# Optimization experiments

Hardware: AMD Instinct MI355X
Metric: run time of the kernel (lower is better)

The kernel has to match this reference:

```python
import jax, jax.numpy as jnp
import numpy as np

N = 100000
NUM_CLASSES = 10
EPS = 1e-16
NEG_SLOPE = 0.2


def gat_conv(x, src, dst, W, a_src, a_dst, bias, heads, out_ch, concat):
    # x: [N, F_in]; src/dst: [E] (message flows src -> dst, PyG convention)
    n = x.shape[0]
    h = (x @ W).reshape(n, heads, out_ch)              # [N, H, C]
    al = jnp.sum(h * a_src, axis=-1)                   # [N, H] source attention term
    ar = jnp.sum(h * a_dst, axis=-1)                   # [N, H] target attention term
    e = jax.nn.leaky_relu(al[src] + ar[dst], NEG_SLOPE)  # [E, H]
    # segment softmax over incoming edges of each dst node
    m = jax.ops.segment_max(e, dst, num_segments=n)    # [N, H]
    ex = jnp.exp(e - m[dst])                           # [E, H]
    denom = jax.ops.segment_sum(ex, dst, num_segments=n)  # [N, H]
    alpha = ex / (denom[dst] + EPS)                    # [E, H]
    msg = h[src] * alpha[..., None]                    # [E, H, C]
    out = jax.ops.segment_sum(msg, dst, num_segments=n)   # [N, H, C]
    out = out.reshape(n, heads * out_ch) if concat else out.mean(axis=1)
    return out + bias


def setup_inputs() -> dict:
    key = jax.random.key(0)
    ks = jax.random.split(key, 10)
    F_in, H1, C1 = 512, 8, 8
    x = jax.random.normal(ks[0], (N, F_in), dtype=jnp.float32)
    edge_index = jax.random.randint(ks[1], (2, 1600000), 0, N, dtype=jnp.int64)
    s = 0.05
    return {
        "x": x,
        "edge_index": edge_index,
        "W1": jax.random.normal(ks[2], (F_in, H1 * C1), dtype=jnp.float32) * s,
        "a_src1": jax.random.normal(ks[3], (H1, C1), dtype=jnp.float32) * s,
        "a_dst1": jax.random.normal(ks[4], (H1, C1), dtype=jnp.float32) * s,
        "b1": jnp.zeros((H1 * C1,), dtype=jnp.float32),
        "W2": jax.random.normal(ks[5], (H1 * C1, NUM_CLASSES), dtype=jnp.float32) * s,
        "a_src2": jax.random.normal(ks[6], (1, NUM_CLASSES), dtype=jnp.float32) * s,
        "a_dst2": jax.random.normal(ks[7], (1, NUM_CLASSES), dtype=jnp.float32) * s,
        "b2": jnp.zeros((NUM_CLASSES,), dtype=jnp.float32),
    }


def reference(x, edge_index, W1, a_src1, a_dst1, b1, W2, a_src2, a_dst2, b2):
    # add self-loops (GATConv default add_self_loops=True)
    loops = jnp.arange(N, dtype=edge_index.dtype)
    src = jnp.concatenate([edge_index[0], loops])
    dst = jnp.concatenate([edge_index[1], loops])
    # eval mode: dropout(p=0.6) is identity
    h = gat_conv(x, src, dst, W1, a_src1, a_dst1, b1, heads=8, out_ch=8, concat=True)
    h = jax.nn.elu(h)
    out = gat_conv(h, src, dst, W2, a_src2, a_dst2, b2, heads=1, out_ch=NUM_CLASSES, concat=True)
    return jax.nn.log_softmax(out, axis=1)
```

## Files before the change

kernel.cpp:

```cpp
#include <hip/hip_runtime.h>
#include <math.h>

#define NN 100000
#define NEDGE 1600000
#define NTOT 1700000
#define FIN 512
#define NH1 8
#define NC1 8
#define F1 64
#define NC2 10
#define SLOPE 0.2f
#define EPSF 1e-16f
#define SCAN_BLK 1024
#define NB ((NN + SCAN_BLK - 1) / SCAN_BLK)

typedef short short8 __attribute__((ext_vector_type(8)));
typedef float f32x4 __attribute__((ext_vector_type(4)));

__device__ __forceinline__ float lrelu(float x) { return x > 0.f ? x : SLOPE * x; }
__device__ __forceinline__ float eluf(float x) { return x > 0.f ? x : __expf(x) - 1.f; }

__device__ __forceinline__ unsigned short f2bf_rne(float f) {
    unsigned int u = __float_as_uint(f);
    unsigned int r = (u + 0x7FFFu + ((u >> 16) & 1u)) >> 16;
    return (unsigned short)r;
}
__device__ __forceinline__ float bf2f(unsigned short b) {
    return __uint_as_float(((unsigned int)b) << 16);
}

__global__ void k_init(const float* __restrict__ W, unsigned short* __restrict__ wT,
                       int* __restrict__ cnt)
{
    int i = blockIdx.x * 256 + threadIdx.x;
    if (i < NN) cnt[i] = 1;
    if (i < F1 * FIN) {
        int n = i & 63, k = i >> 6;
        wT[n * FIN + k] = f2bf_rne(W[k * F1 + n]);
    }
}

#define LDA 40

__global__ __launch_bounds__(256) void k_gemm1(const float* __restrict__ x,
                                               const unsigned short* __restrict__ wT,
                                               const float* __restrict__ asrc,
                                               const float* __restrict__ adst,
                                               unsigned short* __restrict__ h1b,
                                               float* __restrict__ al,
                                               float* __restrict__ ar)
{
    __shared__ unsigned short Al[64][LDA];
    __shared__ unsigned short Bl[64][LDA];
    __shared__ float sas[F1], sad[F1];
    const int tid = threadIdx.x;
    const int row0 = blockIdx.x * 64;
    const int w  = tid >> 6;
    const int l  = tid & 63;
    const int lr = l & 15;
    const int lg = l >> 4;
    if (tid < F1) { sas[tid] = asrc[tid]; sad[tid] = adst[tid]; }
    f32x4 acc[4] = {};

    for (int k0 = 0; k0 < FIN; k0 += 32) {
        #pragma unroll
        for (int t2 = 0; t2 < 2; ++t2) {
            int idx = tid + t2 * 256;
            int r = idx >> 3, q = idx & 7;
            int gr = row0 + r;
            float4 v = (gr < NN) ? *(const float4*)(x + (size_t)gr * FIN + k0 + 4 * q)
                                 : make_float4(0.f, 0.f, 0.f, 0.f);
            ushort4 u;
            u.x = f2bf_rne(v.x); u.y = f2bf_rne(v.y);
            u.z = f2bf_rne(v.z); u.w = f2bf_rne(v.w);
            *(ushort4*)&Al[r][4 * q] = u;
        }
        {
            int n = tid >> 2, q = tid & 3;
            *(uint4*)&Bl[n][8 * q] = *(const uint4*)(wT + (size_t)n * FIN + k0 + 8 * q);
        }
        __syncthreads();
        short8 a = *(const short8*)&Al[16 * w + lr][8 * lg];
        #pragma unroll
        for (int nt = 0; nt < 4; ++nt) {
            short8 b = *(const short8*)&Bl[16 * nt + lr][8 * lg];
            acc[nt] = __builtin_amdgcn_mfma_f32_16x16x32_bf16(a, b, acc[nt], 0, 0, 0);
        }
        __syncthreads();
    }
    #pragma unroll
    for (int r = 0; r < 4; ++r) {
        int gr = row0 + 16 * w + 4 * lg + r;
        if (gr < NN) {
            #pragma unroll
            for (int nt = 0; nt < 4; ++nt)
                h1b[(size_t)gr * F1 + 16 * nt + lr] = f2bf_rne(acc[nt][r]);
        }
    }
    float pa[4][4], pd[4][4];
    #pragma unroll
    for (int nt = 0; nt < 4; ++nt) {
        float wa = sas[16 * nt + lr], wd = sad[16 * nt + lr];
        #pragma unroll
        for (int r = 0; r < 4; ++r) {
            float c = acc[nt][r];
            pa[nt][r] = c * wa;
            pd[nt][r] = c * wd;
        }
    }
    #pragma unroll
    for (int d = 1; d <= 4; d <<= 1) {
        #pragma unroll
        for (int nt = 0; nt < 4; ++nt)
            #pragma unroll
            for (int r = 0; r < 4; ++r) {
                pa[nt][r] += __shfl_xor(pa[nt][r], d);
                pd[nt][r] += __shfl_xor(pd[nt][r], d);
            }
    }
    int low3 = lr & 7, hi = lr >> 3;
    if (low3 < 4) {
        int head = 2 * low3 + hi;
        #pragma unroll
        for (int nt = 0; nt < 4; ++nt) {
            if (low3 == nt) {
                #pragma unroll
                for (int r = 0; r < 4; ++r) {
                    int gr = row0 + 16 * w + 4 * lg + r;
                    if (gr < NN) {
                        al[gr * NH1 + head] = pa[nt][r];
                        ar[gr * NH1 + head] = pd[nt][r];
                    }
                }
            }
        }
    }
}

__global__ void k_hist(const int* __restrict__ ei, int* __restrict__ cnt,
                       int* __restrict__ pos)
{
    int e = blockIdx.x * blockDim.x + threadIdx.x;
    if (e >= NEDGE) return;
    pos[e] = atomicAdd(&cnt[ei[NEDGE + e]], 1);
}

__global__ __launch_bounds__(256) void k_scan1(const int* __restrict__ cnt,
                                               int* __restrict__ off,
                                               int* __restrict__ bsum)
{
    __shared__ int s[256];
    int t = threadIdx.x;
    int base = blockIdx.x * SCAN_BLK + t * 4;
    int c0 = (base + 0 < NN) ? cnt[base + 0] : 0;
    int c1 = (base + 1 < NN) ? cnt[base + 1] : 0;
    int c2 = (base + 2 < NN) ? cnt[base + 2] : 0;
    int c3 = (base + 3 < NN) ? cnt[base + 3] : 0;
    int ts = c0 + c1 + c2 + c3;
    s[t] = ts;
    __syncthreads();
    #pragma unroll
    for (int d = 1; d < 256; d <<= 1) {
        int v = (t >= d) ? s[t - d] : 0;
        __syncthreads();
        s[t] += v;
        __syncthreads();
    }
    int run = s[t] - ts;
    if (t == 255) bsum[blockIdx.x] = s[255];
    if (base + 0 < NN) off[base + 0] = run; run += c0;
    if (base + 1 < NN) off[base + 1] = run; run += c1;
    if (base + 2 < NN) off[base + 2] = run; run += c2;
    if (base + 3 < NN) off[base + 3] = run;
}

__global__ void k_scan2(int* __restrict__ bsum, int* __restrict__ off)
{
    __shared__ int s[128];
    int t = threadIdx.x;
    int v = (t < NB) ? bsum[t] : 0;
    s[t] = v;
    __syncthreads();
    #pragma unroll
    for (int d = 1; d < 128; d <<= 1) {
        int w = (t >= d) ? s[t - d] : 0;
        __syncthreads();
        s[t] += w;
        __syncthreads();
    }
    if (t < NB) bsum[t] = s[t] - v;
    if (t == 0) off[NN] = NTOT;
}

__global__ void k_scan3(int* __restrict__ off, const int* __restrict__ bsum,
                        int* __restrict__ esrc)
{
    int i = blockIdx.x * blockDim.x + threadIdx.x;
    if (i >= NN) return;
    int o = off[i] + bsum[i >> 10];
    off[i] = o;
    esrc[o] = i;
}

__global__ void k_scatter(const int* __restrict__ ei, const int* __restrict__ off,
                          const int* __restrict__ pos, int* __restrict__ esrc)
{
    int e = blockIdx.x * blockDim.x + threadIdx.x;
    if (e >= NEDGE) return;
    esrc[off[ei[NEDGE + e]] + pos[e]] = ei[e];
}

__global__ __launch_bounds__(256) void k_agg1(const int* __restrict__ off,
                                              const int* __restrict__ esrc,
                                              const float* __restrict__ al,
                                              const float* __restrict__ ar,
                                              const unsigned short* __restrict__ h1b,
                                              const float* __restrict__ b1,
                                              const float* __restrict__ W2,
                                              const float* __restrict__ as2,
                                              const float* __restrict__ ad2,
                                              float* __restrict__ packed)
{
    __shared__ float s2a[NC2], s2d[NC2];
    int tid = threadIdx.x;
    if (tid < NC2) { s2a[tid] = as2[tid]; s2d[tid] = ad2[tid]; }
    __syncthreads();
    int node = blockIdx.x * 4 + (tid >> 6);
    int lane = tid & 63;
    int h = lane >> 3;
    float b1l = b1[lane];
    float w2r[NC2];
    #pragma unroll
    for (int o = 0; o < NC2; ++o) w2r[o] = W2[lane * NC2 + o];

    int beg = off[node], end = off[node + 1];
    float arn = ar[node * NH1 + h];
    float a0 = 0.f, a1 = 0.f, a2 = 0.f, a3 = 0.f;
    float d0 = 0.f, d1 = 0.f, d2 = 0.f, d3 = 0.f;
    int i = beg;
    for (; i + 3 < end; i += 4) {
        int s0 = esrc[i], s1 = esrc[i + 1], s2 = esrc[i + 2], s3 = esrc[i + 3];
        float e0 = __expf(lrelu(al[s0 * NH1 + h] + arn));
        float e1 = __expf(lrelu(al[s1 * NH1 + h] + arn));
        float e2 = __expf(lrelu(al[s2 * NH1 + h] + arn));
        float e3 = __expf(lrelu(al[s3 * NH1 + h] + arn));
        a0 += bf2f(h1b[(size_t)s0 * F1 + lane]) * e0; d0 += e0;
        a1 += bf2f(h1b[(size_t)s1 * F1 + lane]) * e1; d1 += e1;
        a2 += bf2f(h1b[(size_t)s2 * F1 + lane]) * e2; d2 += e2;
        a3 += bf2f(h1b[(size_t)s3 * F1 + lane]) * e3; d3 += e3;
    }
    for (; i < end; ++i) {
        int s0 = esrc[i];
        float e0 = __expf(lrelu(al[s0 * NH1 + h] + arn));
        a0 += bf2f(h1b[(size_t)s0 * F1 + lane]) * e0; d0 += e0;
    }
    float v = ((a0 + a1) + (a2 + a3)) / (((d0 + d1) + (d2 + d3)) + EPSF);
    float gl = eluf(v + b1l);

    float p[NC2];
    #pragma unroll
    for (int o = 0; o < NC2; ++o) p[o] = gl * w2r[o];
    #pragma unroll
    for (int d = 1; d <= 32; d <<= 1)
        #pragma unroll
        for (int o = 0; o < NC2; ++o) p[o] += __shfl_xor(p[o], d);
    float sa = 0.f, sd = 0.f;
    #pragma unroll
    for (int o = 0; o < NC2; ++o) { sa += p[o] * s2a[o]; sd += p[o] * s2d[o]; }

    float* rec = packed + (size_t)node * 16;
    if (lane < NC2) rec[lane] = p[lane];
    if (lane == 10) rec[10] = sa;
    if (lane == 11) rec[11] = sd;
}

__global__ __launch_bounds__(256) void k_agg2(const int* __restrict__ off,
                                              const int* __restrict__ esrc,
                                              const float* __restrict__ packed,
                                              const float* __restrict__ b2,
                                              float* __restrict__ out)
{
    int node = blockIdx.x * 16 + (threadIdx.x >> 4);
    int li = threadIdx.x & 15;
    int beg = off[node], end = off[node + 1];
    float arn = packed[(size_t)node * 16 + 11];
    float acc = 0.f, acc1 = 0.f, dsum = 0.f, dsum1 = 0.f;
    int i = beg;
    for (; i + 1 < end; i += 2) {
        int s0 = esrc[i], s1 = esrc[i + 1];
        float v0 = (li < 12) ? packed[(size_t)s0 * 16 + li] : 0.f;
        float v1 = (li < 12) ? packed[(size_t)s1 * 16 + li] : 0.f;
        float al0 = __shfl(v0, 10, 16);
        float al1 = __shfl(v1, 10, 16);
        float e0 = __expf(lrelu(al0 + arn));
        float e1 = __expf(lrelu(al1 + arn));
        if (li < NC2) { acc += v0 * e0; acc1 += v1 * e1; }
        dsum += e0; dsum1 += e1;
    }
    if (i < end) {
        int s0 = esrc[i];
        float v0 = (li < 12) ? packed[(size_t)s0 * 16 + li] : 0.f;
        float al0 = __shfl(v0, 10, 16);
        float e0 = __expf(lrelu(al0 + arn));
        if (li < NC2) acc += v0 * e0;
        dsum += e0;
    }
    float z = (li < NC2) ? (acc + acc1) / (dsum + dsum1 + EPSF) + b2[li] : -1e30f;
    float m = z;
    #pragma unroll
    for (int d = 8; d >= 1; d >>= 1) m = fmaxf(m, __shfl_xor(m, d, 16));
    float ex = (li < NC2) ? __expf(z - m) : 0.f;
    float ss = ex;
    #pragma unroll
    for (int d = 8; d >= 1; d >>= 1) ss += __shfl_xor(ss, d, 16);
    float ls = __logf(ss) + m;
    if (li < NC2) out[(size_t)node * NC2 + li] = z - ls;
}

extern "C" void kernel_launch(void* const* d_in, const int* in_sizes, int n_in,
                              void* d_out, int out_size, void* d_ws, size_t ws_size,
                              hipStream_t stream)
{
    const float* x    = (const float*)d_in[0];
    const int*   ei   = (const int*)d_in[1];
    const float* W1   = (const float*)d_in[2];
    const float* as1  = (const float*)d_in[3];
    const float* ad1  = (const float*)d_in[4];
    const float* b1   = (const float*)d_in[5];
    const float* W2   = (const float*)d_in[6];
    const float* as2  = (const float*)d_in[7];
    const float* ad2  = (const float*)d_in[8];
    const float* b2   = (const float*)d_in[9];
    float* out = (float*)d_out;

    char* ws = (char*)d_ws;
    unsigned short* h1b = (unsigned short*)ws;
    unsigned short* wT  = h1b + (size_t)NN * F1;
    float* al1 = (float*)(wT + (size_t)F1 * FIN);
    float* ar1 = al1 + (size_t)NN * NH1;
    float* packed = ar1 + (size_t)NN * NH1;
    int* cnt   = (int*)(packed + (size_t)NN * 16);
    int* off   = cnt + NN;
    int* bsum  = off + NN + 1;
    int* esrc  = bsum + 128;
    int* pos   = esrc + NTOT;

    k_init<<<(NN + 255) / 256, 256, 0, stream>>>(W1, wT, cnt);
    k_gemm1<<<(NN + 63) / 64, 256, 0, stream>>>(x, wT, as1, ad1, h1b, al1, ar1);
    k_hist<<<(NEDGE + 255) / 256, 256, 0, stream>>>(ei, cnt, pos);
    k_scan1<<<NB, 256, 0, stream>>>(cnt, off, bsum);
    k_scan2<<<1, 128, 0, stream>>>(bsum, off);
    k_scan3<<<(NN + 255) / 256, 256, 0, stream>>>(off, bsum, esrc);
    k_scatter<<<(NEDGE + 255) / 256, 256, 0, stream>>>(ei, off, pos, esrc);
    k_agg1<<<NN / 4, 256, 0, stream>>>(off, esrc, al1, ar1, h1b, b1, W2, as2, ad2, packed);
    k_agg2<<<NN / 16, 256, 0, stream>>>(off, esrc, packed, b2, out);
}
```

Before: 596.1 us.

## Split edge lists across four sub-groups per wavefront in both aggregation kernels

```diff
diff --git a/kernel.cpp b/kernel.cpp
--- a/kernel.cpp
+++ b/kernel.cpp
@@ -221,49 +221,58 @@
                                               const float* __restrict__ ad2,
                                               float* __restrict__ packed)
 {
+    __shared__ float sW[F1 * NC2];
+    __shared__ float sb1[F1];
     __shared__ float s2a[NC2], s2d[NC2];
     int tid = threadIdx.x;
+    for (int i = tid; i < F1 * NC2; i += 256) sW[i] = W2[i];
+    if (tid < F1) sb1[tid] = b1[tid];
     if (tid < NC2) { s2a[tid] = as2[tid]; s2d[tid] = ad2[tid]; }
     __syncthreads();
+
     int node = blockIdx.x * 4 + (tid >> 6);
     int lane = tid & 63;
-    int h = lane >> 3;
-    float b1l = b1[lane];
-    float w2r[NC2];
-    #pragma unroll
-    for (int o = 0; o < NC2; ++o) w2r[o] = W2[lane * NC2 + o];
-
+    int sub  = lane >> 4;
+    int li   = lane & 15;
+    int head = li >> 1;
     int beg = off[node], end = off[node + 1];
-    float arn = ar[node * NH1 + h];
-    float a0 = 0.f, a1 = 0.f, a2 = 0.f, a3 = 0.f;
-    float d0 = 0.f, d1 = 0.f, d2 = 0.f, d3 = 0.f;
-    int i = beg;
-    for (; i + 3 < end; i += 4) {
-        int s0 = esrc[i], s1 = esrc[i + 1], s2 = esrc[i + 2], s3 = esrc[i + 3];
-        float e0 = __expf(lrelu(al[s0 * NH1 + h] + arn));
-        float e1 = __expf(lrelu(al[s1 * NH1 + h] + arn));
-        float e2 = __expf(lrelu(al[s2 * NH1 + h] + arn));
-        float e3 = __expf(lrelu(al[s3 * NH1 + h] + arn));
-        a0 += bf2f(h1b[(size_t)s0 * F1 + lane]) * e0; d0 += e0;
-        a1 += bf2f(h1b[(size_t)s1 * F1 + lane]) * e1; d1 += e1;
-        a2 += bf2f(h1b[(size_t)s2 * F1 + lane]) * e2; d2 += e2;
-        a3 += bf2f(h1b[(size_t)s3 * F1 + lane]) * e3; d3 += e3;
-    }
-    for (; i < end; ++i) {
-        int s0 = esrc[i];
-        float e0 = __expf(lrelu(al[s0 * NH1 + h] + arn));
-        a0 += bf2f(h1b[(size_t)s0 * F1 + lane]) * e0; d0 += e0;
-    }
-    float v = ((a0 + a1) + (a2 + a3)) / (((d0 + d1) + (d2 + d3)) + EPSF);
-    float gl = eluf(v + b1l);
+    float arn = ar[node * NH1 + head];
+
+    float a0 = 0.f, a1 = 0.f, a2 = 0.f, a3 = 0.f, ds = 0.f;
+    for (int i = beg + sub; i < end; i += 4) {
+        int s = esrc[i];
+        float e = __expf(lrelu(al[s * NH1 + head] + arn));
+        ushort4 hv = *(const ushort4*)(h1b + (size_t)s * F1 + 4 * li);
+        a0 += bf2f(hv.x) * e;
+        a1 += bf2f(hv.y) * e;
+        a2 += bf2f(hv.z) * e;
+        a3 += bf2f(hv.w) * e;
+        ds += e;
+    }
+    #pragma unroll
+    for (int d = 16; d <= 32; d <<= 1) {
+        a0 += __shfl_xor(a0, d);
+        a1 += __shfl_xor(a1, d);
+        a2 += __shfl_xor(a2, d);
+        a3 += __shfl_xor(a3, d);
+        ds += __shfl_xor(ds, d);
+    }
+    float inv = 1.f / (ds + EPSF);
+    float g0 = eluf(a0 * inv + sb1[4 * li + 0]);
+    float g1 = eluf(a1 * inv + sb1[4 * li + 1]);
+    float g2 = eluf(a2 * inv + sb1[4 * li + 2]);
+    float g3 = eluf(a3 * inv + sb1[4 * li + 3]);
 
     float p[NC2];
     #pragma unroll
-    for (int o = 0; o < NC2; ++o) p[o] = gl * w2r[o];
-    #pragma unroll
-    for (int d = 1; d <= 32; d <<= 1)
+    for (int o = 0; o < NC2; ++o)
+        p[o] = g0 * sW[(4 * li + 0) * NC2 + o] + g1 * sW[(4 * li + 1) * NC2 + o]
+             + g2 * sW[(4 * li + 2) * NC2 + o] + g3 * sW[(4 * li + 3) * NC2 + o];
+    #pragma unroll
+    for (int d = 1; d <= 8; d <<= 1)
         #pragma unroll
         for (int o = 0; o < NC2; ++o) p[o] += __shfl_xor(p[o], d);
+
     float sa = 0.f, sd = 0.f;
     #pragma unroll
     for (int o = 0; o < NC2; ++o) { sa += p[o] * s2a[o]; sd += p[o] * s2d[o]; }
@@ -280,32 +289,29 @@
                                               const float* __restrict__ b2,
                                               float* __restrict__ out)
 {
-    int node = blockIdx.x * 16 + (threadIdx.x >> 4);
-    int li = threadIdx.x & 15;
+    int tid = threadIdx.x;
+    int node = blockIdx.x * 4 + (tid >> 6);
+    int lane = tid & 63;
+    int sub  = lane >> 4;
+    int li   = lane & 15;
     int beg = off[node], end = off[node + 1];
     float arn = packed[(size_t)node * 16 + 11];
-    float acc = 0.f, acc1 = 0.f, dsum = 0.f, dsum1 = 0.f;
-    int i = beg;
-    for (; i + 1 < end; i += 2) {
-        int s0 = esrc[i], s1 = esrc[i + 1];
-        float v0 = (li < 12) ? packed[(size_t)s0 * 16 + li] : 0.f;
-        float v1 = (li < 12) ? packed[(size_t)s1 * 16 + li] : 0.f;
-        float al0 = __shfl(v0, 10, 16);
-        float al1 = __shfl(v1, 10, 16);
-        float e0 = __expf(lrelu(al0 + arn));
-        float e1 = __expf(lrelu(al1 + arn));
-        if (li < NC2) { acc += v0 * e0; acc1 += v1 * e1; }
-        dsum += e0; dsum1 += e1;
-    }
-    if (i < end) {
-        int s0 = esrc[i];
-        float v0 = (li < 12) ? packed[(size_t)s0 * 16 + li] : 0.f;
-        float al0 = __shfl(v0, 10, 16);
-        float e0 = __expf(lrelu(al0 + arn));
-        if (li < NC2) acc += v0 * e0;
-        dsum += e0;
-    }
-    float z = (li < NC2) ? (acc + acc1) / (dsum + dsum1 + EPSF) + b2[li] : -1e30f;
+
+    float acc = 0.f, ds = 0.f;
+    for (int i = beg + sub; i < end; i += 4) {
+        int s = esrc[i];
+        float v = (li < 12) ? packed[(size_t)s * 16 + li] : 0.f;
+        float al2s = __shfl(v, 10, 16);
+        float e = __expf(lrelu(al2s + arn));
+        if (li < NC2) acc += v * e;
+        ds += e;
+    }
+    #pragma unroll
+    for (int d = 16; d <= 32; d <<= 1) {
+        acc += __shfl_xor(acc, d);
+        ds  += __shfl_xor(ds, d);
+    }
+    float z = (li < NC2) ? acc / (ds + EPSF) + b2[li] : -1e30f;
     float m = z;
     #pragma unroll
     for (int d = 8; d >= 1; d >>= 1) m = fmaxf(m, __shfl_xor(m, d, 16));
@@ -314,7 +320,7 @@
     #pragma unroll
     for (int d = 8; d >= 1; d >>= 1) ss += __shfl_xor(ss, d, 16);
     float ls = __logf(ss) + m;
-    if (li < NC2) out[(size_t)node * NC2 + li] = z - ls;
+    if (lane < NC2) out[(size_t)node * NC2 + lane] = z - ls;
 }
 
 extern "C" void kernel_launch(void* const* d_in, const int* in_sizes, int n_in,
@@ -353,5 +359,5 @@
     k_scan3<<<(NN + 255) / 256, 256, 0, stream>>>(off, bsum, esrc);
     k_scatter<<<(NEDGE + 255) / 256, 256, 0, stream>>>(ei, off, pos, esrc);
     k_agg1<<<NN / 4, 256, 0, stream>>>(off, esrc, al1, ar1, h1b, b1, W2, as2, ad2, packed);
-    k_agg2<<<NN / 16, 256, 0, stream>>>(off, esrc, packed, b2, out);
-}
+    k_agg2<<<NN / 4, 256, 0, stream>>>(off, esrc, packed, b2, out);
+}
```

Result: slower. 613.0 us (+2.8%).
